# Kernel tuning notes

Measured on AMD Instinct MI355X. Metric: run time of the kernel, lower is better.

## Reference

```python
import jax, jax.numpy as jnp
import numpy as np

N = 8192      # atoms
B = 64        # molecules
E = 262144    # edges
S = 4         # species
NMAX = 8      # radial basis size
CUT = 5.0     # cutoff radius
AVG_ATOMS = 128.0
E_SCALE = 1.0
PS_DIM = (S * NMAX) ** 2 * 4  # l_max=3 -> 4 l channels -> 4096
H1, H2 = 1024, 1024
OUT = 1


def _sph_harm(u):
    # real spherical harmonics up to l=3, input unit vectors [E,3] -> [E,16]
    x, y, z = u[:, 0], u[:, 1], u[:, 2]
    x2, y2, z2 = x * x, y * y, z * z
    return jnp.stack([
        0.28209479 * jnp.ones_like(x),
        0.48860251 * y, 0.48860251 * z, 0.48860251 * x,
        1.09254843 * x * y, 1.09254843 * y * z, 0.31539157 * (3.0 * z2 - 1.0),
        1.09254843 * x * z, 0.54627422 * (x2 - y2),
        0.59004359 * y * (3.0 * x2 - y2), 2.89061144 * x * y * z,
        0.45704579 * y * (5.0 * z2 - 1.0), 0.37317633 * z * (5.0 * z2 - 3.0),
        0.45704579 * x * (5.0 * z2 - 1.0), 1.44530572 * z * (x2 - y2),
        0.59004359 * x * (x2 - 3.0 * y2),
    ], axis=-1)


def setup_inputs() -> dict:
    key = jax.random.key(0)
    ks = jax.random.split(key, 12)
    positions = jax.random.normal(ks[0], (N, 3), dtype=jnp.float32) * 1.5  # dense cloud so many pairs < CUT
    cells = jnp.tile(20.0 * jnp.eye(3, dtype=jnp.float32)[None], (B, 1, 1))
    numbers = jax.random.randint(ks[1], (N,), 0, S)
    edge_indices = jax.random.randint(ks[2], (2, E), 0, N)
    edge_offsets = jnp.zeros((E, 3), dtype=jnp.float32)
    batch = jnp.arange(N) // (N // B)
    gamma = 1.0 + 0.1 * jax.random.normal(ks[3], (PS_DIM,), dtype=jnp.float32)
    beta = 0.1 * jax.random.normal(ks[4], (PS_DIM,), dtype=jnp.float32)
    W_ps = jax.random.normal(ks[5], (PS_DIM, OUT), dtype=jnp.float32) / np.sqrt(PS_DIM)
    W1 = jax.random.normal(ks[6], (PS_DIM, H1), dtype=jnp.float32) / np.sqrt(PS_DIM)
    W2 = jax.random.normal(ks[7], (H1, H2), dtype=jnp.float32) / np.sqrt(H1)
    W3 = jax.random.normal(ks[8], (H2, OUT), dtype=jnp.float32) / np.sqrt(H2)
    W_comp = jax.random.normal(ks[9], (S, OUT), dtype=jnp.float32) / np.sqrt(S)
    return dict(positions=positions, cells=cells, numbers=numbers,
                edge_indices=edge_indices, edge_offsets=edge_offsets, batch=batch,
                gamma=gamma, beta=beta, W_ps=W_ps, W1=W1, W2=W2, W3=W3, W_comp=W_comp)


def reference(positions, cells, numbers, edge_indices, edge_offsets, batch,
              gamma, beta, W_ps, W1, W2, W3, W_comp):
    i, j = edge_indices[0], edge_indices[1]  # center, neighbor
    # periodic shift: fractional offsets through the cell of the center's molecule
    shift = jnp.einsum('ec,ecd->ed', edge_offsets, cells[batch[i]])
    rvec = positions[j] - positions[i] + shift                      # [E,3]
    r = jnp.sqrt(jnp.sum(rvec * rvec, axis=-1) + 1e-12)             # [E]
    u = rvec / r[:, None]
    fc = 0.5 * (jnp.cos(jnp.pi * jnp.minimum(r, CUT) / CUT) + 1.0) * (r < CUT)
    n = jnp.arange(1, NMAX + 1, dtype=positions.dtype)
    R = fc[:, None] * jnp.sin(jnp.pi * n[None, :] * r[:, None] / CUT) / r[:, None]  # [E,NMAX]
    Y = _sph_harm(u)                                                # [E,16]
    edge_feat = R[:, :, None] * Y[:, None, :]                       # [E,NMAX,16]
    # spherical expansion c[i, species(j), n, lm] via scatter-add
    seg = i * S + numbers[j]
    c = jax.ops.segment_sum(edge_feat, seg, num_segments=N * S)     # [N*S,NMAX,16]
    c = c.reshape(N, S * NMAX, 16)
    # power spectrum: contract over m within each l block
    bounds = [(0, 1), (1, 4), (4, 9), (9, 16)]
    p = [jnp.einsum('ixm,iym->ixy', c[:, :, s:e], c[:, :, s:e]) for s, e in bounds]
    ps = jnp.stack(p, axis=-1).reshape(N, PS_DIM)                   # [N,4096]
    # LayerNorm (eps=1e-5, affine)
    mu = jnp.mean(ps, axis=-1, keepdims=True)
    var = jnp.var(ps, axis=-1, keepdims=True)
    psn = (ps - mu) / jnp.sqrt(var + 1e-5) * gamma + beta
    # linear branch + MLP branch
    psl = psn @ W_ps                                                # [N,1]
    h = jax.nn.silu(psn @ W1)
    h = jax.nn.silu(h @ W2)
    psnn = h @ W3                                                   # [N,1]
    # pool atomic energies into per-molecule totals (index_add)
    energies = jax.ops.segment_sum(psl + psnn, batch, num_segments=B) / AVG_ATOMS
    # eval path: composition baseline
    comp = jax.ops.segment_sum(jax.nn.one_hot(numbers, S, dtype=psn.dtype), batch, num_segments=B)
    return energies * E_SCALE + comp @ W_comp                       # [B,1]
```

## Files before the change

kernel.cpp:

```cpp
#include <hip/hip_runtime.h>
#include <hip/hip_bf16.h>
#include <math.h>

#define N_ATOMS 8192
#define B_BATCH 64
#define E_EDGES 262144
#define S_SPEC 4
#define NMAX 8
#define PS_DIM 4096
#define H1_DIM 1024
#define CAP4 48
#define CUTR 5.0f
#define PI_F 3.14159265358979f

typedef __bf16 bf16;
typedef bf16 bf16x8 __attribute__((ext_vector_type(8)));
typedef float floatx4 __attribute__((ext_vector_type(4)));
typedef int intx8 __attribute__((ext_vector_type(8)));
typedef unsigned char u8;

__device__ __forceinline__ void g2lds16(const void* g, void* l) {
    __builtin_amdgcn_global_load_lds(
        (const __attribute__((address_space(1))) void*)g,
        (__attribute__((address_space(3))) void*)l, 16, 0, 0);
}

__device__ __forceinline__ int pk_fp8x4(float a, float b, float c, float d) {
    int lo = __builtin_amdgcn_cvt_pk_fp8_f32(a, b, 0, false);
    return __builtin_amdgcn_cvt_pk_fp8_f32(c, d, lo, true);
}

__global__ __launch_bounds__(256) void scatter_kernel(
    const float* __restrict__ pos, const float* __restrict__ cells,
    const int* __restrict__ numbers, const int* __restrict__ ei,
    const float* __restrict__ eo, const int* __restrict__ batch,
    int* __restrict__ cnt, float4* __restrict__ bucket)
{
    int e = blockIdx.x * 256 + threadIdx.x;
    int i = ei[e];
    int j = ei[E_EDGES + e];
    int b = batch[i];
    const float* cell = cells + b * 9;
    float o0 = eo[e * 3 + 0], o1 = eo[e * 3 + 1], o2 = eo[e * 3 + 2];
    float rv[3];
    #pragma unroll
    for (int d = 0; d < 3; ++d) {
        float shift = o0 * cell[0 * 3 + d] + o1 * cell[1 * 3 + d] + o2 * cell[2 * 3 + d];
        rv[d] = pos[j * 3 + d] - pos[i * 3 + d] + shift;
    }
    float r2 = rv[0] * rv[0] + rv[1] * rv[1] + rv[2] * rv[2] + 1e-12f;
    if (r2 >= CUTR * CUTR) return;
    float r = sqrtf(r2);
    float a1 = r * (PI_F / CUTR);
    int sp = numbers[j];
    int q = i * S_SPEC + sp;
    int slot = atomicAdd(&cnt[q], 1);
    if (slot < CAP4)
        bucket[q * CAP4 + slot] = make_float4(rv[0], rv[1], rv[2], a1);
}

__global__ __launch_bounds__(256) void accum_kernel(
    const float4* __restrict__ bucket, const int* __restrict__ cnt,
    float* __restrict__ c)
{
    int wv = threadIdx.x >> 6, lane = threadIdx.x & 63;
    int atom = blockIdx.x * 4 + wv;

    int sp_l = lane >> 4;
    float nf = (float)(((lane >> 1) & 7) + 1);
    int par = lane & 1;

    int myCnt = cnt[atom * S_SPEC + sp_l];
    if (myCnt > CAP4) myCnt = CAP4;
    int m1 = max(myCnt, __shfl_xor(myCnt, 16));
    int mx = max(m1, __shfl_xor(m1, 32));

    const float4* q = bucket + (size_t)(atom * S_SPEC + sp_l) * CAP4;
    float acc[8] = {};
    #pragma unroll 2
    for (int e = 0; e < mx; ++e) {
        float4 d = q[e];
        bool valid = e < myCnt;
        float a1 = d.w;
        float inv_r = (PI_F / CUTR) * __frcp_rn(a1);
        float fc = 0.5f * __cosf(a1) + 0.5f;
        float rn = fc * inv_r * __sinf(nf * a1);
        rn = valid ? rn : 0.0f;

        float x = d.x * inv_r, y = d.y * inv_r, z = d.z * inv_r;
        float x2 = x * x, y2 = y * y, z2 = z * z;
        float Ys[8];
        if (par == 0) {
            Ys[0] = 0.28209479f;
            Ys[1] = 0.48860251f * y;
            Ys[2] = 0.48860251f * z;
            Ys[3] = 0.48860251f * x;
            Ys[4] = 1.09254843f * x * y;
            Ys[5] = 1.09254843f * y * z;
            Ys[6] = 0.31539157f * (3.0f * z2 - 1.0f);
            Ys[7] = 1.09254843f * x * z;
        } else {
            Ys[0] = 0.54627422f * (x2 - y2);
            Ys[1] = 0.59004359f * y * (3.0f * x2 - y2);
            Ys[2] = 2.89061144f * x * y * z;
            Ys[3] = 0.45704579f * y * (5.0f * z2 - 1.0f);
            Ys[4] = 0.37317633f * z * (5.0f * z2 - 3.0f);
            Ys[5] = 0.45704579f * x * (5.0f * z2 - 1.0f);
            Ys[6] = 1.44530572f * z * (x2 - y2);
            Ys[7] = 0.59004359f * x * (x2 - 3.0f * y2);
        }
        #pragma unroll
        for (int k = 0; k < 8; ++k) acc[k] += rn * Ys[k];
    }

    float* dst = c + (size_t)atom * 512 + lane * 8;
    *(float4*)(dst + 0) = make_float4(acc[0], acc[1], acc[2], acc[3]);
    *(float4*)(dst + 4) = make_float4(acc[4], acc[5], acc[6], acc[7]);
}

__global__ __launch_bounds__(256) void transpose_convert2(
    const float* __restrict__ W1, u8* __restrict__ Wt1,
    const float* __restrict__ W2, u8* __restrict__ Wt2)
{
    const float* W; u8* Wt; int K; float scale; int bx;
    if (blockIdx.x < 128) { W = W1; Wt = Wt1; K = PS_DIM; scale = 64.0f; bx = blockIdx.x; }
    else                  { W = W2; Wt = Wt2; K = H1_DIM; scale = 32.0f; bx = blockIdx.x - 128; }
    const int Nc = H1_DIM;
    __shared__ float t[32][33];
    int k0 = bx * 32, n0 = blockIdx.y * 32;
    int tx = threadIdx.x & 31, ty = threadIdx.x >> 5;
    #pragma unroll
    for (int r = 0; r < 32; r += 8)
        t[ty + r][tx] = W[(size_t)(k0 + ty + r) * Nc + n0 + tx];
    __syncthreads();
    if (threadIdx.x < 64) {
        int nl = threadIdx.x >> 1, cc = threadIdx.x & 1;
        int n = n0 + nl;
        unsigned int w[4];
        #pragma unroll
        for (int g = 0; g < 4; ++g) {
            int kb = cc * 16 + g * 4;
            w[g] = (unsigned int)pk_fp8x4(
                t[kb + 0][nl] * scale, t[kb + 1][nl] * scale,
                t[kb + 2][nl] * scale, t[kb + 3][nl] * scale);
        }
        int gc = (k0 >> 4) + cc;
        int gcs = (gc & ~7) | ((gc & 7) ^ (n & 7));
        *(uint4*)(Wt + (size_t)n * K + (size_t)gcs * 16) = make_uint4(w[0], w[1], w[2], w[3]);
    }
}

__global__ __launch_bounds__(256) void atom_ps_kernel(
    const float* __restrict__ c, const float* __restrict__ gamma,
    const float* __restrict__ beta, const float* __restrict__ Wps,
    u8* __restrict__ psn, float* __restrict__ psl)
{
    int atom = blockIdx.x;
    int t = threadIdx.x;
    __shared__ __align__(16) float cl_x[32 * 20];
    __shared__ __align__(16) u8 ps_s8[PS_DIM];
    __shared__ float red[8];
    __shared__ float red2[4];

    const float* ca = c + (size_t)atom * 512;
    {
        float2 v = ((const float2*)ca)[t];
        int x0 = t >> 3;
        int m0 = (t & 7) * 2;
        cl_x[x0 * 20 + m0] = v.x;
        cl_x[x0 * 20 + m0 + 1] = v.y;
    }
    __syncthreads();

    int y = t & 31;
    int xb = t >> 5;
    float4 cya = *(const float4*)&cl_x[y * 20 + 0];
    float4 cyb = *(const float4*)&cl_x[y * 20 + 4];
    float4 cyc = *(const float4*)&cl_x[y * 20 + 8];
    float4 cyd = *(const float4*)&cl_x[y * 20 + 12];

    float ps[4][4];
    float sum = 0.0f, sumsq = 0.0f;
    #pragma unroll
    for (int q = 0; q < 4; ++q) {
        int x = xb + 8 * q;
        float4 xa = *(const float4*)&cl_x[x * 20 + 0];
        float4 xbv = *(const float4*)&cl_x[x * 20 + 4];
        float4 xc = *(const float4*)&cl_x[x * 20 + 8];
        float4 xd = *(const float4*)&cl_x[x * 20 + 12];
        float s0 = xa.x * cya.x;
        float s1 = xa.y * cya.y + xa.z * cya.z + xa.w * cya.w;
        float s2 = xbv.x * cyb.x + xbv.y * cyb.y + xbv.z * cyb.z + xbv.w * cyb.w
                 + xc.x * cyc.x;
        float s3 = xc.y * cyc.y + xc.z * cyc.z + xc.w * cyc.w
                 + xd.x * cyd.x + xd.y * cyd.y + xd.z * cyd.z + xd.w * cyd.w;
        ps[q][0] = s0; ps[q][1] = s1; ps[q][2] = s2; ps[q][3] = s3;
        sum += s0 + s1 + s2 + s3;
        sumsq += s0 * s0 + s1 * s1 + s2 * s2 + s3 * s3;
    }
    #pragma unroll
    for (int o = 32; o > 0; o >>= 1) {
        sum += __shfl_down(sum, o);
        sumsq += __shfl_down(sumsq, o);
    }
    int wv = t >> 6;
    if ((t & 63) == 0) { red[wv] = sum; red[4 + wv] = sumsq; }
    __syncthreads();
    float tot = red[0] + red[1] + red[2] + red[3];
    float totsq = red[4] + red[5] + red[6] + red[7];
    float mu = tot * (1.0f / PS_DIM);
    float var = totsq * (1.0f / PS_DIM) - mu * mu;
    float inv = rsqrtf(var + 1e-5f);

    float pacc = 0.0f;
    #pragma unroll
    for (int q = 0; q < 4; ++q) {
        int p = t + 256 * q;
        float4 g = *(const float4*)(gamma + p * 4);
        float4 bt = *(const float4*)(beta + p * 4);
        float4 w = *(const float4*)(Wps + p * 4);
        float v0 = (ps[q][0] - mu) * inv * g.x + bt.x;
        float v1 = (ps[q][1] - mu) * inv * g.y + bt.y;
        float v2 = (ps[q][2] - mu) * inv * g.z + bt.z;
        float v3 = (ps[q][3] - mu) * inv * g.w + bt.w;
        pacc += v0 * w.x + v1 * w.y + v2 * w.z + v3 * w.w;
        ((int*)ps_s8)[p] = pk_fp8x4(v0, v1, v2, v3);
    }
    __syncthreads();
    u8* rowp = psn + (size_t)atom * PS_DIM;
    int key = atom & 7;
    int gcs = (t & ~7) | ((t & 7) ^ key);
    *(uint4*)(rowp + (size_t)gcs * 16) = *(const uint4*)(ps_s8 + (size_t)t * 16);

    #pragma unroll
    for (int o = 32; o > 0; o >>= 1) pacc += __shfl_down(pacc, o);
    if ((t & 63) == 0) red2[wv] = pacc;
    __syncthreads();
    if (t == 0) psl[atom] = red2[0] + red2[1] + red2[2] + red2[3];
}

template<int OUT_FP8>
__global__ __launch_bounds__(256) void gemm_f8_kernel(
    const u8* __restrict__ A, const u8* __restrict__ Bt,
    void* __restrict__ H, int M, int Nc, int K, float invs)
{
    __shared__ __align__(16) char smem[24576];
    int tid = threadIdx.x;
    int bm = blockIdx.x, bn = blockIdx.y;
    int wave = tid >> 6, lane = tid & 63;
    int wm = (wave >> 1) * 32, wn = (wave & 1) * 64;
    int lm = lane & 15, quad = lane >> 4;

    floatx4 acc[2][4] = {};
    const int rowA0 = bm * 64, rowB0 = bn * 128;
    const size_t stride = (size_t)K;
    const char* Ab = (const char*)A + (size_t)rowA0 * stride;
    const char* Bb = (const char*)Bt + (size_t)rowB0 * stride;
    const int sA = 0x7F7F7F7F, sB = 0x7F7F7F7F;

    for (int k0 = 0; k0 < K; k0 += 128) {
        #pragma unroll
        for (int s = 0; s < 2; ++s) {
            int L = s * 256 + tid;
            int row = L >> 3, boff = (L & 7) * 16;
            int lbase = (s * 256 + wave * 64) * 16;
            g2lds16(Ab + (size_t)row * stride + k0 + boff, smem + lbase);
        }
        #pragma unroll
        for (int s = 0; s < 4; ++s) {
            int L = s * 256 + tid;
            int row = L >> 3, boff = (L & 7) * 16;
            int lbase = (s * 256 + wave * 64) * 16;
            g2lds16(Bb + (size_t)row * stride + k0 + boff, smem + 8192 + lbase);
        }
        __syncthreads();
        int key = lm & 7;
        int c0 = (2 * quad) ^ key, c1 = (2 * quad + 1) ^ key;
        intx8 af[2], bfr[4];
        #pragma unroll
        for (int mi = 0; mi < 2; ++mi) {
            const char* base = smem + (wm + mi * 16 + lm) * 128;
            uint4 lo = *(const uint4*)(base + c0 * 16);
            uint4 hi = *(const uint4*)(base + c1 * 16);
            af[mi][0] = lo.x; af[mi][1] = lo.y; af[mi][2] = lo.z; af[mi][3] = lo.w;
            af[mi][4] = hi.x; af[mi][5] = hi.y; af[mi][6] = hi.z; af[mi][7] = hi.w;
        }
        #pragma unroll
        for (int ni = 0; ni < 4; ++ni) {
            const char* base = smem + 8192 + (wn + ni * 16 + lm) * 128;
            uint4 lo = *(const uint4*)(base + c0 * 16);
            uint4 hi = *(const uint4*)(base + c1 * 16);
            bfr[ni][0] = lo.x; bfr[ni][1] = lo.y; bfr[ni][2] = lo.z; bfr[ni][3] = lo.w;
            bfr[ni][4] = hi.x; bfr[ni][5] = hi.y; bfr[ni][6] = hi.z; bfr[ni][7] = hi.w;
        }
        #pragma unroll
        for (int mi = 0; mi < 2; ++mi)
            #pragma unroll
            for (int ni = 0; ni < 4; ++ni)
                acc[mi][ni] = __builtin_amdgcn_mfma_scale_f32_16x16x128_f8f6f4(
                    af[mi], bfr[ni], acc[mi][ni], 0, 0, 0, sA, 0, sB);
        __syncthreads();
    }

    if (OUT_FP8) {
        u8* Cs8 = (u8*)smem;
        #pragma unroll
        for (int mi = 0; mi < 2; ++mi)
            #pragma unroll
            for (int ni = 0; ni < 4; ++ni)
                #pragma unroll
                for (int r = 0; r < 4; ++r) {
                    int row = wm + mi * 16 + quad * 4 + r;
                    int col = wn + ni * 16 + lm;
                    float v = acc[mi][ni][r] * invs;
                    v = v / (1.0f + __expf(-v));
                    int pk = __builtin_amdgcn_cvt_pk_fp8_f32(v, 0.0f, 0, false);
                    Cs8[row * 128 + col] = (u8)(pk & 0xFF);
                }
        __syncthreads();
        #pragma unroll
        for (int c2 = 0; c2 < 2; ++c2) {
            int L = c2 * 256 + tid;
            int row = L >> 3, cc = L & 7;
            int gcs = cc ^ (row & 7);
            *(uint4*)((u8*)H + (size_t)(rowA0 + row) * Nc + (size_t)(bn * 8 + gcs) * 16) =
                *(const uint4*)(Cs8 + (size_t)L * 16);
        }
    } else {
        bf16* Cs = (bf16*)smem;
        #pragma unroll
        for (int mi = 0; mi < 2; ++mi)
            #pragma unroll
            for (int ni = 0; ni < 4; ++ni)
                #pragma unroll
                for (int r = 0; r < 4; ++r) {
                    int row = wm + mi * 16 + quad * 4 + r;
                    int col = wn + ni * 16 + lm;
                    float v = acc[mi][ni][r] * invs;
                    v = v / (1.0f + __expf(-v));
                    Cs[row * 128 + col] = (bf16)v;
                }
        __syncthreads();
        const size_t strideH = (size_t)Nc * 2;
        #pragma unroll
        for (int c2 = 0; c2 < 4; ++c2) {
            int L = c2 * 256 + tid;
            int row = L >> 4, cc = L & 15;
            *(uint4*)((char*)H + (size_t)(rowA0 + row) * strideH + (size_t)(bn * 16 + cc) * 16) =
                *(const uint4*)((char*)Cs + (size_t)L * 16);
        }
    }
}

__global__ __launch_bounds__(256) void tail_kernel(
    const bf16* __restrict__ h2, const float* __restrict__ W3,
    const float* __restrict__ psl, const int* __restrict__ numbers,
    const float* __restrict__ Wcomp, float* __restrict__ out)
{
    int b = blockIdx.x;
    int t = threadIdx.x;
    int wv = t >> 6, lane = t & 63;
    __shared__ float tot;
    __shared__ int cnt4[S_SPEC];
    if (t == 0) tot = 0.0f;
    if (t < S_SPEC) cnt4[t] = 0;
    __syncthreads();

    if (t < 128) {
        int a = b * 128 + t;
        atomicAdd(&tot, psl[a]);
        atomicAdd(&cnt4[numbers[a]], 1);
    }

    float acc = 0.0f;
    for (int k = 0; k < 32; ++k) {
        int atom = b * 128 + wv * 32 + k;
        const bf16* h = h2 + (size_t)atom * H1_DIM;
        #pragma unroll
        for (int q2 = 0; q2 < 2; ++q2) {
            int k0 = (lane + 64 * q2) * 8;
            bf16x8 hv = *(const bf16x8*)(h + k0);
            float4 w0 = *(const float4*)(W3 + k0);
            float4 w1 = *(const float4*)(W3 + k0 + 4);
            acc += (float)hv[0] * w0.x + (float)hv[1] * w0.y
                 + (float)hv[2] * w0.z + (float)hv[3] * w0.w
                 + (float)hv[4] * w1.x + (float)hv[5] * w1.y
                 + (float)hv[6] * w1.z + (float)hv[7] * w1.w;
        }
    }
    #pragma unroll
    for (int o = 32; o > 0; o >>= 1) acc += __shfl_down(acc, o);
    if (lane == 0) atomicAdd(&tot, acc);
    __syncthreads();
    if (t == 0) {
        float r = tot * (1.0f / 128.0f);
        #pragma unroll
        for (int s = 0; s < S_SPEC; ++s) r += (float)cnt4[s] * Wcomp[s];
        out[b] = r;
    }
}

extern "C" void kernel_launch(void* const* d_in, const int* in_sizes, int n_in,
                              void* d_out, int out_size, void* d_ws, size_t ws_size,
                              hipStream_t stream)
{
    const float* positions = (const float*)d_in[0];
    const float* cells     = (const float*)d_in[1];
    const int*   numbers   = (const int*)d_in[2];
    const int*   ei        = (const int*)d_in[3];
    const float* eo        = (const float*)d_in[4];
    const int*   batch     = (const int*)d_in[5];
    const float* gamma     = (const float*)d_in[6];
    const float* beta      = (const float*)d_in[7];
    const float* W_ps      = (const float*)d_in[8];
    const float* W1        = (const float*)d_in[9];
    const float* W2        = (const float*)d_in[10];
    const float* W3        = (const float*)d_in[11];
    const float* W_comp    = (const float*)d_in[12];
    float* out = (float*)d_out;

    char* ws = (char*)d_ws;
    float* c    = (float*)ws;  ws += (size_t)N_ATOMS * 512 * 4;
    u8*    psn  = (u8*)ws;     ws += (size_t)N_ATOMS * PS_DIM;
    u8*    h1   = (u8*)ws;     ws += (size_t)N_ATOMS * H1_DIM;
    bf16*  h2   = (bf16*)ws;   ws += (size_t)N_ATOMS * H1_DIM * 2;
    u8*    Wt1  = (u8*)ws;     ws += (size_t)H1_DIM * PS_DIM;
    u8*    Wt2  = (u8*)ws;     ws += (size_t)H1_DIM * H1_DIM;
    float* psl  = (float*)ws;  ws += (size_t)N_ATOMS * 4;
    float* e_at = (float*)ws;  ws += (size_t)N_ATOMS * 4;

    float4* bucket = (float4*)psn;
    int* cnt = (int*)h1;

    hipMemsetAsync(cnt, 0, N_ATOMS * S_SPEC * sizeof(int), stream);

    scatter_kernel<<<E_EDGES / 256, 256, 0, stream>>>(
        positions, cells, numbers, ei, eo, batch, cnt, bucket);
    accum_kernel<<<N_ATOMS / 4, 256, 0, stream>>>(bucket, cnt, c);

    transpose_convert2<<<dim3(160, 32), 256, 0, stream>>>(W1, Wt1, W2, Wt2);

    atom_ps_kernel<<<N_ATOMS, 256, 0, stream>>>(c, gamma, beta, W_ps, psn, psl);

    gemm_f8_kernel<1><<<dim3(N_ATOMS / 64, H1_DIM / 128), 256, 0, stream>>>(
        psn, Wt1, (void*)h1, N_ATOMS, H1_DIM, PS_DIM, 1.0f / 64.0f);
    gemm_f8_kernel<0><<<dim3(N_ATOMS / 64, H1_DIM / 128), 256, 0, stream>>>(
        h1, Wt2, (void*)h2, N_ATOMS, H1_DIM, H1_DIM, 1.0f / 32.0f);

    tail_kernel<<<B_BATCH, 256, 0, stream>>>(h2, W3, psl, numbers, W_comp, out);
}
```

Before: 226.2 us.

## Load GEMM A fragments directly from global and shrink the LDS footprint

The fp8 GEMM no longer stages the A tile through LDS. Each wave reads its A fragments straight from global memory into registers, using the existing swizzled layout, while only B goes through LDS via global_load_lds. That cuts LDS use from 24 KB to 16 KB per block, which may raise occupancy and removes LDS round-trips for A, at the cost of less coalesced, duplicated A loads from global. The epilogue is also unified: results always go to LDS as bf16 and are converted to fp8 on write-out, which adds a double rounding step.

```diff
diff --git a/kernel.cpp b/kernel.cpp
--- a/kernel.cpp
+++ b/kernel.cpp
@@ -244,7 +244,7 @@
     const u8* __restrict__ A, const u8* __restrict__ Bt,
     void* __restrict__ H, int M, int Nc, int K, float invs)
 {
-    __shared__ __align__(16) char smem[24576];
+    __shared__ __align__(16) char smem[16384];
     int tid = threadIdx.x;
     int bm = blockIdx.x, bn = blockIdx.y;
     int wave = tid >> 6, lane = tid & 63;
@@ -258,36 +258,31 @@
     const char* Bb = (const char*)Bt + (size_t)rowB0 * stride;
     const int sA = 0x7F7F7F7F, sB = 0x7F7F7F7F;
 
+    int key = lm & 7;
+    int c0 = (2 * quad) ^ key, c1 = (2 * quad + 1) ^ key;
+
     for (int k0 = 0; k0 < K; k0 += 128) {
-        #pragma unroll
-        for (int s = 0; s < 2; ++s) {
-            int L = s * 256 + tid;
-            int row = L >> 3, boff = (L & 7) * 16;
-            int lbase = (s * 256 + wave * 64) * 16;
-            g2lds16(Ab + (size_t)row * stride + k0 + boff, smem + lbase);
-        }
         #pragma unroll
         for (int s = 0; s < 4; ++s) {
             int L = s * 256 + tid;
             int row = L >> 3, boff = (L & 7) * 16;
             int lbase = (s * 256 + wave * 64) * 16;
-            g2lds16(Bb + (size_t)row * stride + k0 + boff, smem + 8192 + lbase);
-        }
-        __syncthreads();
-        int key = lm & 7;
-        int c0 = (2 * quad) ^ key, c1 = (2 * quad + 1) ^ key;
-        intx8 af[2], bfr[4];
+            g2lds16(Bb + (size_t)row * stride + k0 + boff, smem + lbase);
+        }
+        intx8 af[2];
         #pragma unroll
         for (int mi = 0; mi < 2; ++mi) {
-            const char* base = smem + (wm + mi * 16 + lm) * 128;
-            uint4 lo = *(const uint4*)(base + c0 * 16);
-            uint4 hi = *(const uint4*)(base + c1 * 16);
+            const char* ar = Ab + (size_t)(wm + mi * 16 + lm) * stride + k0;
+            uint4 lo = *(const uint4*)(ar + c0 * 16);
+            uint4 hi = *(const uint4*)(ar + c1 * 16);
             af[mi][0] = lo.x; af[mi][1] = lo.y; af[mi][2] = lo.z; af[mi][3] = lo.w;
             af[mi][4] = hi.x; af[mi][5] = hi.y; af[mi][6] = hi.z; af[mi][7] = hi.w;
         }
+        __syncthreads();
+        intx8 bfr[4];
         #pragma unroll
         for (int ni = 0; ni < 4; ++ni) {
-            const char* base = smem + 8192 + (wn + ni * 16 + lm) * 128;
+            const char* base = smem + (wn + ni * 16 + lm) * 128;
             uint4 lo = *(const uint4*)(base + c0 * 16);
             uint4 hi = *(const uint4*)(base + c1 * 16);
             bfr[ni][0] = lo.x; bfr[ni][1] = lo.y; bfr[ni][2] = lo.z; bfr[ni][3] = lo.w;
@@ -302,45 +297,37 @@
         __syncthreads();
     }
 
+    bf16* Cs = (bf16*)smem;
+    #pragma unroll
+    for (int mi = 0; mi < 2; ++mi)
+        #pragma unroll
+        for (int ni = 0; ni < 4; ++ni)
+            #pragma unroll
+            for (int r = 0; r < 4; ++r) {
+                int row = wm + mi * 16 + quad * 4 + r;
+                int col = wn + ni * 16 + lm;
+                float v = acc[mi][ni][r] * invs;
+                v = v / (1.0f + __expf(-v));
+                Cs[row * 128 + col] = (bf16)v;
+            }
+    __syncthreads();
     if (OUT_FP8) {
-        u8* Cs8 = (u8*)smem;
-        #pragma unroll
-        for (int mi = 0; mi < 2; ++mi)
-            #pragma unroll
-            for (int ni = 0; ni < 4; ++ni)
-                #pragma unroll
-                for (int r = 0; r < 4; ++r) {
-                    int row = wm + mi * 16 + quad * 4 + r;
-                    int col = wn + ni * 16 + lm;
-                    float v = acc[mi][ni][r] * invs;
-                    v = v / (1.0f + __expf(-v));
-                    int pk = __builtin_amdgcn_cvt_pk_fp8_f32(v, 0.0f, 0, false);
-                    Cs8[row * 128 + col] = (u8)(pk & 0xFF);
-                }
-        __syncthreads();
         #pragma unroll
         for (int c2 = 0; c2 < 2; ++c2) {
             int L = c2 * 256 + tid;
             int row = L >> 3, cc = L & 7;
+            const bf16* src = Cs + row * 128 + cc * 16;
+            bf16x8 a0 = *(const bf16x8*)(src);
+            bf16x8 a1 = *(const bf16x8*)(src + 8);
+            uint4 o;
+            o.x = (unsigned)pk_fp8x4(a0[0], a0[1], a0[2], a0[3]);
+            o.y = (unsigned)pk_fp8x4(a0[4], a0[5], a0[6], a0[7]);
+            o.z = (unsigned)pk_fp8x4(a1[0], a1[1], a1[2], a1[3]);
+            o.w = (unsigned)pk_fp8x4(a1[4], a1[5], a1[6], a1[7]);
             int gcs = cc ^ (row & 7);
-            *(uint4*)((u8*)H + (size_t)(rowA0 + row) * Nc + (size_t)(bn * 8 + gcs) * 16) =
-                *(const uint4*)(Cs8 + (size_t)L * 16);
+            *(uint4*)((u8*)H + (size_t)(rowA0 + row) * Nc + (size_t)(bn * 8 + gcs) * 16) = o;
         }
     } else {
-        bf16* Cs = (bf16*)smem;
-        #pragma unroll
-        for (int mi = 0; mi < 2; ++mi)
-            #pragma unroll
-            for (int ni = 0; ni < 4; ++ni)
-                #pragma unroll
-                for (int r = 0; r < 4; ++r) {
-                    int row = wm + mi * 16 + quad * 4 + r;
-                    int col = wn + ni * 16 + lm;
-                    float v = acc[mi][ni][r] * invs;
-                    v = v / (1.0f + __expf(-v));
-                    Cs[row * 128 + col] = (bf16)v;
-                }
-        __syncthreads();
         const size_t strideH = (size_t)Nc * 2;
         #pragma unroll
         for (int c2 = 0; c2 < 4; ++c2) {
@@ -427,7 +414,6 @@
     u8*    Wt1  = (u8*)ws;     ws += (size_t)H1_DIM * PS_DIM;
     u8*    Wt2  = (u8*)ws;     ws += (size_t)H1_DIM * H1_DIM;
     float* psl  = (float*)ws;  ws += (size_t)N_ATOMS * 4;
-    float* e_at = (float*)ws;  ws += (size_t)N_ATOMS * 4;
 
     float4* bucket = (float4*)psn;
     int* cnt = (int*)h1;
```

Measured after the change: 233.4 us. +3.2%, slower.

## Fuse radial/angular accumulation with power-spectrum LayerNorm kernel

Applied to the files above, without the earlier changes.

Merges the per-atom density accumulation and the power-spectrum/LayerNorm/linear kernel into one kernel. Each block accumulates coefficients for four atoms straight into shared memory, then loops over those atoms to build the normalized fp8 power spectrum. This removes the global round trip of the c coefficient array and one launch. The bucket and count buffers get their own workspace regions, since the bucket can no longer alias psn while it is still being read. The trade-off is that the power-spectrum phase now runs four atoms serially per block, with extra barriers and fewer blocks.

```diff
diff --git a/kernel.cpp b/kernel.cpp
--- a/kernel.cpp
+++ b/kernel.cpp
@@ -59,63 +59,145 @@
         bucket[q * CAP4 + slot] = make_float4(rv[0], rv[1], rv[2], a1);
 }
 
-__global__ __launch_bounds__(256) void accum_kernel(
+__global__ __launch_bounds__(256) void accum_ps_kernel(
     const float4* __restrict__ bucket, const int* __restrict__ cnt,
-    float* __restrict__ c)
-{
-    int wv = threadIdx.x >> 6, lane = threadIdx.x & 63;
-    int atom = blockIdx.x * 4 + wv;
-
-    int sp_l = lane >> 4;
-    float nf = (float)(((lane >> 1) & 7) + 1);
-    int par = lane & 1;
-
-    int myCnt = cnt[atom * S_SPEC + sp_l];
-    if (myCnt > CAP4) myCnt = CAP4;
-    int m1 = max(myCnt, __shfl_xor(myCnt, 16));
-    int mx = max(m1, __shfl_xor(m1, 32));
-
-    const float4* q = bucket + (size_t)(atom * S_SPEC + sp_l) * CAP4;
-    float acc[8] = {};
-    #pragma unroll 2
-    for (int e = 0; e < mx; ++e) {
-        float4 d = q[e];
-        bool valid = e < myCnt;
-        float a1 = d.w;
-        float inv_r = (PI_F / CUTR) * __frcp_rn(a1);
-        float fc = 0.5f * __cosf(a1) + 0.5f;
-        float rn = fc * inv_r * __sinf(nf * a1);
-        rn = valid ? rn : 0.0f;
-
-        float x = d.x * inv_r, y = d.y * inv_r, z = d.z * inv_r;
-        float x2 = x * x, y2 = y * y, z2 = z * z;
-        float Ys[8];
-        if (par == 0) {
-            Ys[0] = 0.28209479f;
-            Ys[1] = 0.48860251f * y;
-            Ys[2] = 0.48860251f * z;
-            Ys[3] = 0.48860251f * x;
-            Ys[4] = 1.09254843f * x * y;
-            Ys[5] = 1.09254843f * y * z;
-            Ys[6] = 0.31539157f * (3.0f * z2 - 1.0f);
-            Ys[7] = 1.09254843f * x * z;
-        } else {
-            Ys[0] = 0.54627422f * (x2 - y2);
-            Ys[1] = 0.59004359f * y * (3.0f * x2 - y2);
-            Ys[2] = 2.89061144f * x * y * z;
-            Ys[3] = 0.45704579f * y * (5.0f * z2 - 1.0f);
-            Ys[4] = 0.37317633f * z * (5.0f * z2 - 3.0f);
-            Ys[5] = 0.45704579f * x * (5.0f * z2 - 1.0f);
-            Ys[6] = 1.44530572f * z * (x2 - y2);
-            Ys[7] = 0.59004359f * x * (x2 - 3.0f * y2);
-        }
-        #pragma unroll
-        for (int k = 0; k < 8; ++k) acc[k] += rn * Ys[k];
-    }
-
-    float* dst = c + (size_t)atom * 512 + lane * 8;
-    *(float4*)(dst + 0) = make_float4(acc[0], acc[1], acc[2], acc[3]);
-    *(float4*)(dst + 4) = make_float4(acc[4], acc[5], acc[6], acc[7]);
+    const float* __restrict__ gamma, const float* __restrict__ beta,
+    const float* __restrict__ Wps, u8* __restrict__ psn, float* __restrict__ psl)
+{
+    __shared__ __align__(16) float cl[4][32 * 20];
+    __shared__ __align__(16) u8 ps_s8[PS_DIM];
+    __shared__ float red[8];
+    __shared__ float red2[4];
+
+    int t = threadIdx.x;
+    int wv = t >> 6, lane = t & 63;
+    int atom0 = blockIdx.x * 4;
+
+    {
+        int atom = atom0 + wv;
+        int sp_l = lane >> 4;
+        int nidx = (lane >> 1) & 7;
+        float nf = (float)(nidx + 1);
+        int par = lane & 1;
+
+        int myCnt = cnt[atom * S_SPEC + sp_l];
+        if (myCnt > CAP4) myCnt = CAP4;
+        int m1 = max(myCnt, __shfl_xor(myCnt, 16));
+        int mx = max(m1, __shfl_xor(m1, 32));
+
+        const float4* q = bucket + (size_t)(atom * S_SPEC + sp_l) * CAP4;
+        float acc[8] = {};
+        #pragma unroll 2
+        for (int e = 0; e < mx; ++e) {
+            float4 d = q[e];
+            bool valid = e < myCnt;
+            float a1 = d.w;
+            float inv_r = (PI_F / CUTR) * __frcp_rn(a1);
+            float fc = 0.5f * __cosf(a1) + 0.5f;
+            float rn = fc * inv_r * __sinf(nf * a1);
+            rn = valid ? rn : 0.0f;
+
+            float x = d.x * inv_r, y = d.y * inv_r, z = d.z * inv_r;
+            float x2 = x * x, y2 = y * y, z2 = z * z;
+            float Ys[8];
+            if (par == 0) {
+                Ys[0] = 0.28209479f;
+                Ys[1] = 0.48860251f * y;
+                Ys[2] = 0.48860251f * z;
+                Ys[3] = 0.48860251f * x;
+                Ys[4] = 1.09254843f * x * y;
+                Ys[5] = 1.09254843f * y * z;
+                Ys[6] = 0.31539157f * (3.0f * z2 - 1.0f);
+                Ys[7] = 1.09254843f * x * z;
+            } else {
+                Ys[0] = 0.54627422f * (x2 - y2);
+                Ys[1] = 0.59004359f * y * (3.0f * x2 - y2);
+                Ys[2] = 2.89061144f * x * y * z;
+                Ys[3] = 0.45704579f * y * (5.0f * z2 - 1.0f);
+                Ys[4] = 0.37317633f * z * (5.0f * z2 - 3.0f);
+                Ys[5] = 0.45704579f * x * (5.0f * z2 - 1.0f);
+                Ys[6] = 1.44530572f * z * (x2 - y2);
+                Ys[7] = 0.59004359f * x * (x2 - 3.0f * y2);
+            }
+            #pragma unroll
+            for (int k = 0; k < 8; ++k) acc[k] += rn * Ys[k];
+        }
+        int X = sp_l * 8 + nidx;
+        float* dst = &cl[wv][X * 20 + par * 8];
+        *(float4*)(dst + 0) = make_float4(acc[0], acc[1], acc[2], acc[3]);
+        *(float4*)(dst + 4) = make_float4(acc[4], acc[5], acc[6], acc[7]);
+    }
+    __syncthreads();
+
+    for (int a = 0; a < 4; ++a) {
+        int atom = atom0 + a;
+        const float* cl_x = cl[a];
+
+        int y = t & 31;
+        int xb = t >> 5;
+        float4 cya = *(const float4*)&cl_x[y * 20 + 0];
+        float4 cyb = *(const float4*)&cl_x[y * 20 + 4];
+        float4 cyc = *(const float4*)&cl_x[y * 20 + 8];
+        float4 cyd = *(const float4*)&cl_x[y * 20 + 12];
+
+        float ps[4][4];
+        float sum = 0.0f, sumsq = 0.0f;
+        #pragma unroll
+        for (int q = 0; q < 4; ++q) {
+            int x = xb + 8 * q;
+            float4 xa = *(const float4*)&cl_x[x * 20 + 0];
+            float4 xbv = *(const float4*)&cl_x[x * 20 + 4];
+            float4 xc = *(const float4*)&cl_x[x * 20 + 8];
+            float4 xd = *(const float4*)&cl_x[x * 20 + 12];
+            float s0 = xa.x * cya.x;
+            float s1 = xa.y * cya.y + xa.z * cya.z + xa.w * cya.w;
+            float s2 = xbv.x * cyb.x + xbv.y * cyb.y + xbv.z * cyb.z + xbv.w * cyb.w
+                     + xc.x * cyc.x;
+            float s3 = xc.y * cyc.y + xc.z * cyc.z + xc.w * cyc.w
+                     + xd.x * cyd.x + xd.y * cyd.y + xd.z * cyd.z + xd.w * cyd.w;
+            ps[q][0] = s0; ps[q][1] = s1; ps[q][2] = s2; ps[q][3] = s3;
+            sum += s0 + s1 + s2 + s3;
+            sumsq += s0 * s0 + s1 * s1 + s2 * s2 + s3 * s3;
+        }
+        #pragma unroll
+        for (int o = 32; o > 0; o >>= 1) {
+            sum += __shfl_down(sum, o);
+            sumsq += __shfl_down(sumsq, o);
+        }
+        if ((t & 63) == 0) { red[wv] = sum; red[4 + wv] = sumsq; }
+        __syncthreads();
+        float tot = red[0] + red[1] + red[2] + red[3];
+        float totsq = red[4] + red[5] + red[6] + red[7];
+        float mu = tot * (1.0f / PS_DIM);
+        float var = totsq * (1.0f / PS_DIM) - mu * mu;
+        float inv = rsqrtf(var + 1e-5f);
+
+        float pacc = 0.0f;
+        #pragma unroll
+        for (int q = 0; q < 4; ++q) {
+            int p = t + 256 * q;
+            float4 g = *(const float4*)(gamma + p * 4);
+            float4 bt = *(const float4*)(beta + p * 4);
+            float4 w = *(const float4*)(Wps + p * 4);
+            float v0 = (ps[q][0] - mu) * inv * g.x + bt.x;
+            float v1 = (ps[q][1] - mu) * inv * g.y + bt.y;
+            float v2 = (ps[q][2] - mu) * inv * g.z + bt.z;
+            float v3 = (ps[q][3] - mu) * inv * g.w + bt.w;
+            pacc += v0 * w.x + v1 * w.y + v2 * w.z + v3 * w.w;
+            ((int*)ps_s8)[p] = pk_fp8x4(v0, v1, v2, v3);
+        }
+        __syncthreads();
+        u8* rowp = psn + (size_t)atom * PS_DIM;
+        int key = atom & 7;
+        int gcs = (t & ~7) | ((t & 7) ^ key);
+        *(uint4*)(rowp + (size_t)gcs * 16) = *(const uint4*)(ps_s8 + (size_t)t * 16);
+
+        #pragma unroll
+        for (int o = 32; o > 0; o >>= 1) pacc += __shfl_down(pacc, o);
+        if ((t & 63) == 0) red2[wv] = pacc;
+        __syncthreads();
+        if (t == 0) psl[atom] = red2[0] + red2[1] + red2[2] + red2[3];
+    }
 }
 
 __global__ __launch_bounds__(256) void transpose_convert2(
@@ -150,95 +232,6 @@
     }
 }
 
-__global__ __launch_bounds__(256) void atom_ps_kernel(
-    const float* __restrict__ c, const float* __restrict__ gamma,
-    const float* __restrict__ beta, const float* __restrict__ Wps,
-    u8* __restrict__ psn, float* __restrict__ psl)
-{
-    int atom = blockIdx.x;
-    int t = threadIdx.x;
-    __shared__ __align__(16) float cl_x[32 * 20];
-    __shared__ __align__(16) u8 ps_s8[PS_DIM];
-    __shared__ float red[8];
-    __shared__ float red2[4];
-
-    const float* ca = c + (size_t)atom * 512;
-    {
-        float2 v = ((const float2*)ca)[t];
-        int x0 = t >> 3;
-        int m0 = (t & 7) * 2;
-        cl_x[x0 * 20 + m0] = v.x;
-        cl_x[x0 * 20 + m0 + 1] = v.y;
-    }
-    __syncthreads();
-
-    int y = t & 31;
-    int xb = t >> 5;
-    float4 cya = *(const float4*)&cl_x[y * 20 + 0];
-    float4 cyb = *(const float4*)&cl_x[y * 20 + 4];
-    float4 cyc = *(const float4*)&cl_x[y * 20 + 8];
-    float4 cyd = *(const float4*)&cl_x[y * 20 + 12];
-
-    float ps[4][4];
-    float sum = 0.0f, sumsq = 0.0f;
-    #pragma unroll
-    for (int q = 0; q < 4; ++q) {
-        int x = xb + 8 * q;
-        float4 xa = *(const float4*)&cl_x[x * 20 + 0];
-        float4 xbv = *(const float4*)&cl_x[x * 20 + 4];
-        float4 xc = *(const float4*)&cl_x[x * 20 + 8];
-        float4 xd = *(const float4*)&cl_x[x * 20 + 12];
-        float s0 = xa.x * cya.x;
-        float s1 = xa.y * cya.y + xa.z * cya.z + xa.w * cya.w;
-        float s2 = xbv.x * cyb.x + xbv.y * cyb.y + xbv.z * cyb.z + xbv.w * cyb.w
-                 + xc.x * cyc.x;
-        float s3 = xc.y * cyc.y + xc.z * cyc.z + xc.w * cyc.w
-                 + xd.x * cyd.x + xd.y * cyd.y + xd.z * cyd.z + xd.w * cyd.w;
-        ps[q][0] = s0; ps[q][1] = s1; ps[q][2] = s2; ps[q][3] = s3;
-        sum += s0 + s1 + s2 + s3;
-        sumsq += s0 * s0 + s1 * s1 + s2 * s2 + s3 * s3;
-    }
-    #pragma unroll
-    for (int o = 32; o > 0; o >>= 1) {
-        sum += __shfl_down(sum, o);
-        sumsq += __shfl_down(sumsq, o);
-    }
-    int wv = t >> 6;
-    if ((t & 63) == 0) { red[wv] = sum; red[4 + wv] = sumsq; }
-    __syncthreads();
-    float tot = red[0] + red[1] + red[2] + red[3];
-    float totsq = red[4] + red[5] + red[6] + red[7];
-    float mu = tot * (1.0f / PS_DIM);
-    float var = totsq * (1.0f / PS_DIM) - mu * mu;
-    float inv = rsqrtf(var + 1e-5f);
-
-    float pacc = 0.0f;
-    #pragma unroll
-    for (int q = 0; q < 4; ++q) {
-        int p = t + 256 * q;
-        float4 g = *(const float4*)(gamma + p * 4);
-        float4 bt = *(const float4*)(beta + p * 4);
-        float4 w = *(const float4*)(Wps + p * 4);
-        float v0 = (ps[q][0] - mu) * inv * g.x + bt.x;
-        float v1 = (ps[q][1] - mu) * inv * g.y + bt.y;
-        float v2 = (ps[q][2] - mu) * inv * g.z + bt.z;
-        float v3 = (ps[q][3] - mu) * inv * g.w + bt.w;
-        pacc += v0 * w.x + v1 * w.y + v2 * w.z + v3 * w.w;
-        ((int*)ps_s8)[p] = pk_fp8x4(v0, v1, v2, v3);
-    }
-    __syncthreads();
-    u8* rowp = psn + (size_t)atom * PS_DIM;
-    int key = atom & 7;
-    int gcs = (t & ~7) | ((t & 7) ^ key);
-    *(uint4*)(rowp + (size_t)gcs * 16) = *(const uint4*)(ps_s8 + (size_t)t * 16);
-
-    #pragma unroll
-    for (int o = 32; o > 0; o >>= 1) pacc += __shfl_down(pacc, o);
-    if ((t & 63) == 0) red2[wv] = pacc;
-    __syncthreads();
-    if (t == 0) psl[atom] = red2[0] + red2[1] + red2[2] + red2[3];
-}
-
 template<int OUT_FP8>
 __global__ __launch_bounds__(256) void gemm_f8_kernel(
     const u8* __restrict__ A, const u8* __restrict__ Bt,
@@ -420,27 +413,24 @@
     float* out = (float*)d_out;
 
     char* ws = (char*)d_ws;
-    float* c    = (float*)ws;  ws += (size_t)N_ATOMS * 512 * 4;
+    float4* bucket = (float4*)ws;  ws += (size_t)N_ATOMS * S_SPEC * CAP4 * 16;
     u8*    psn  = (u8*)ws;     ws += (size_t)N_ATOMS * PS_DIM;
     u8*    h1   = (u8*)ws;     ws += (size_t)N_ATOMS * H1_DIM;
     bf16*  h2   = (bf16*)ws;   ws += (size_t)N_ATOMS * H1_DIM * 2;
     u8*    Wt1  = (u8*)ws;     ws += (size_t)H1_DIM * PS_DIM;
     u8*    Wt2  = (u8*)ws;     ws += (size_t)H1_DIM * H1_DIM;
     float* psl  = (float*)ws;  ws += (size_t)N_ATOMS * 4;
-    float* e_at = (float*)ws;  ws += (size_t)N_ATOMS * 4;
-
-    float4* bucket = (float4*)psn;
-    int* cnt = (int*)h1;
+    int*   cnt  = (int*)ws;    ws += (size_t)N_ATOMS * S_SPEC * 4;
 
     hipMemsetAsync(cnt, 0, N_ATOMS * S_SPEC * sizeof(int), stream);
 
     scatter_kernel<<<E_EDGES / 256, 256, 0, stream>>>(
         positions, cells, numbers, ei, eo, batch, cnt, bucket);
-    accum_kernel<<<N_ATOMS / 4, 256, 0, stream>>>(bucket, cnt, c);
 
     transpose_convert2<<<dim3(160, 32), 256, 0, stream>>>(W1, Wt1, W2, Wt2);
 
-    atom_ps_kernel<<<N_ATOMS, 256, 0, stream>>>(c, gamma, beta, W_ps, psn, psl);
+    accum_ps_kernel<<<N_ATOMS / 4, 256, 0, stream>>>(
+        bucket, cnt, gamma, beta, W_ps, psn, psl);
 
     gemm_f8_kernel<1><<<dim3(N_ATOMS / 64, H1_DIM / 128), 256, 0, stream>>>(
         psn, Wt1, (void*)h1, N_ATOMS, H1_DIM, PS_DIM, 1.0f / 64.0f);
```

New measurement: 214.0 us. 5.4% less time.
